# Kernel optimization log

Measured on AMD Instinct MI355X. Metric: run time of the kernel, lower is better.

The kernel has to match this reference:

```python
import jax, jax.numpy as jnp
import numpy as np

GRID_NUM = 5   # number of grid intervals (pykan default)
SPLINE_K = 3   # B-spline degree (pykan default)
GRID_RANGE = (-1.0, 1.0)


def make_grid(in_dim):
    # Extended uniform grid: num + 2k + 1 knots per input dim, shared values.
    h = (GRID_RANGE[1] - GRID_RANGE[0]) / GRID_NUM
    pts = GRID_RANGE[0] + h * jnp.arange(-SPLINE_K, GRID_NUM + SPLINE_K + 1, dtype=jnp.float32)
    return jnp.broadcast_to(pts, (in_dim, pts.shape[0]))  # (in_dim, num+2k+1)


def bspline_basis(x, grid, k):
    # Cox-de Boor recursion. x: (n, d); grid: (d, m). Returns (n, d, m-1-k).
    xe = x[..., None]            # (n, d, 1)
    g = grid[None]               # (1, d, m)
    B = ((xe >= g[..., :-1]) & (xe < g[..., 1:])).astype(x.dtype)
    for p in range(1, k + 1):
        left = (xe - g[..., :-(p + 1)]) / (g[..., p:-1] - g[..., :-(p + 1)])
        right = (g[..., p + 1:] - xe) / (g[..., p + 1:] - g[..., 1:-p])
        B = left * B[..., :-1] + right * B[..., 1:]
    return B


def kan_layer(x, coef, scale_base, scale_sp, grid):
    # x: (n, in); coef: (in, out, G+k); scales: (in, out)
    basis = bspline_basis(x, grid, SPLINE_K)              # (n, in, G+k)
    base = jax.nn.silu(x)                                 # (n, in)
    # y[n,o] = sum_i scale_base[i,o]*silu(x[n,i]) + scale_sp[i,o]*sum_g B[n,i,g]*coef[i,o,g]
    spline = jnp.einsum('nig,iog->no', basis, coef * scale_sp[:, :, None])
    return base @ scale_base + spline


def setup_inputs() -> dict:
    key = jax.random.key(0)
    ks = jax.random.split(key, 5)
    b, s, hid, ffn = 2, 4096, 512, 2048
    nb = GRID_NUM + SPLINE_K  # 8 basis functions
    x = jax.random.normal(ks[0], (b, s, hid), dtype=jnp.float32)
    coef1 = 0.1 * jax.random.normal(ks[1], (hid, ffn, nb), dtype=jnp.float32)
    scale_base1 = (1.0 / np.sqrt(hid)) * jax.random.normal(ks[2], (hid, ffn), dtype=jnp.float32)
    scale_sp1 = jnp.ones((hid, ffn), dtype=jnp.float32)
    coef2 = 0.1 * jax.random.normal(ks[3], (ffn, hid, nb), dtype=jnp.float32)
    scale_base2 = (1.0 / np.sqrt(ffn)) * jax.random.normal(ks[4], (ffn, hid), dtype=jnp.float32)
    scale_sp2 = jnp.ones((ffn, hid), dtype=jnp.float32)
    return {'x': x, 'coef1': coef1, 'scale_base1': scale_base1, 'scale_sp1': scale_sp1,
            'coef2': coef2, 'scale_base2': scale_base2, 'scale_sp2': scale_sp2}


def reference(x, coef1, scale_base1, scale_sp1, coef2, scale_base2, scale_sp2):
    b, s, hid = x.shape
    ffn = coef1.shape[1]
    grid1 = make_grid(hid)   # non-trainable buffers, derived from defaults
    grid2 = make_grid(ffn)
    h = x.reshape(b * s, hid)                     # rearrange 'b s h -> (b s) h'
    h = kan_layer(h, coef1, scale_base1, scale_sp1, grid1)
    h = kan_layer(h, coef2, scale_base2, scale_sp2, grid2)
    return h.reshape(b, s, hid)
```

## Files before the change

### kernel.cpp

```cpp
#include <hip/hip_runtime.h>
#include <cstdint>
#include <cstddef>

typedef _Float16 f16;
typedef _Float16 f16x8 __attribute__((ext_vector_type(8)));
typedef float f32x4 __attribute__((ext_vector_type(4)));


template <int I, int O>
__global__ void prep_coef(const float* __restrict__ coef,
                          const float* __restrict__ ssp,
                          f16* __restrict__ Wt) {
  constexpr int K32 = (9 * I) / 32;
  int tid = blockIdx.x * 256 + threadIdx.x;
  if (tid >= I * O) return;
  int i = tid / O, o = tid % O;
  float s = ssp[tid];
  const float* c = coef + (size_t)tid * 8;
  f16x8 out;
#pragma unroll
  for (int g = 0; g < 8; ++g) out[g] = (f16)(c[g] * s);
  size_t addr = ((size_t)(o >> 4) * K32 + (i >> 2)) * 512 +
                (size_t)(((i & 3) * 16) + (o & 15)) * 8;
  *(f16x8*)(Wt + addr) = out;
}

template <int I, int O>
__global__ void prep_base(const float* __restrict__ sb, f16* __restrict__ Wt) {
  constexpr int K32 = (9 * I) / 32;
  int tid = blockIdx.x * 256 + threadIdx.x;
  if (tid >= (I / 8) * O) return;
  int i8 = tid / O, o = tid % O;
  f16x8 out;
#pragma unroll
  for (int s = 0; s < 8; ++s)
    out[s] = (f16)sb[(size_t)(i8 * 8 + s) * O + o];
  size_t addr = ((size_t)(o >> 4) * K32 + (I / 4) + (i8 >> 2)) * 512 +
                (size_t)(((i8 & 3) * 16) + (o & 15)) * 8;
  *(f16x8*)(Wt + addr) = out;
}

__device__ __forceinline__ f16x8 spline8(float h) {
  float v = __builtin_fmaf(2.5f, h, 5.5f);
  float c = floorf(v);
  float f = v - c;
  float f2 = f * f, f3 = f2 * f;
  float b3 = f3 * (1.f / 6.f);
  float t = 1.f - f;
  float b0 = t * t * t * (1.f / 6.f);
  float b1 = (2.f / 3.f) - f2 + 0.5f * f3;
  float b2 = 1.f - b0 - b1 - b3;
  unsigned int u01 =
      __builtin_bit_cast(unsigned int, __builtin_amdgcn_cvt_pkrtz(b0, b1));
  unsigned int u23 =
      __builtin_bit_cast(unsigned int, __builtin_amdgcn_cvt_pkrtz(b2, b3));
  unsigned long long pk = (unsigned long long)u01 |
                          ((unsigned long long)u23 << 32);
  int ci = (int)c;
  int s = (ci - 3) * 16;
  __uint128_t r = 0;
  if (s >= 0) {
    if (s < 128) r = (__uint128_t)pk << s;
  } else {
    int q = -s;
    if (q < 64) r = (__uint128_t)(pk >> q);
  }
  return __builtin_bit_cast(f16x8, r);
}

template <int I, int ATOMIC, int NX, int NZ>
__global__ __launch_bounds__(256, 2) void gemm_kan(const float* __restrict__ H,
                                                   const f16* __restrict__ W,
                                                   float* __restrict__ C,
                                                   int N) {
  constexpr int K = 9 * I;
  constexpr int KB = 8 * I;
  constexpr int K32 = K / 32;
  constexpr int KSTEP = 64 * NZ;
  constexpr int NSTEP = K / KSTEP;
  __shared__ __align__(16) f16 sA[2 * 128 * 64];
  const int t = threadIdx.x;
  const int wg = blockIdx.x;
  const int pr = wg & 7;
  const int n0 = (pr % NX) * 256;
  const int m0 = (wg >> 3) * 128;
  const int kBeg = (pr / NX) * 64;
  const int w = t >> 6, lane = t & 63;
  const int wm = (w >> 1) * 64, wn = (w & 1) * 128;
  const int lr = lane & 15, lq = lane >> 4;
  const int srow = t >> 3;
  const int j_ = t & 7;
  const int js = j_ ^ (srow & 7);

  f32x4 acc[4][8] = {};
  const float* Hrow = H + (size_t)(m0 + srow) * I;

  float hs[4];

  auto genTile = [&](int kg, f16* wb) {
    if (kg < KB) {
#pragma unroll
      for (int q = 0; q < 4; ++q)
        *(f16x8*)&wb[((q * 32 + srow) * 8 + js) * 8] = spline8(hs[q]);
      const int kn = kg + KSTEP;
      if (kn < KB) {
        const int i0n = kn >> 3;
#pragma unroll
        for (int q = 0; q < 4; ++q)
          hs[q] = Hrow[(size_t)(q * 32) * I + i0n + j_];
      }
    } else {
      const int c0 = (kg - KB) + j_ * 8;
      f32x4 ha[4][2];
#pragma unroll
      for (int q = 0; q < 4; ++q) {
        const f32x4* p = (const f32x4*)(Hrow + (size_t)(q * 32) * I + c0);
        ha[q][0] = p[0];
        ha[q][1] = p[1];
      }
#pragma unroll
      for (int q = 0; q < 4; ++q) {
        f16x8 o;
#pragma unroll
        for (int s = 0; s < 8; ++s) {
          float h = ha[q][s >> 2][s & 3];
          o[s] = (f16)(h / (1.f + __expf(-h)));
        }
        *(f16x8*)&wb[((q * 32 + srow) * 8 + js) * 8] = o;
      }
    }
  };

  if (kBeg < KB) {
    const int i0 = kBeg >> 3;
#pragma unroll
    for (int q = 0; q < 4; ++q)
      hs[q] = Hrow[(size_t)(q * 32) * I + i0 + j_];
  }
  const f16* pk = W + ((size_t)((n0 + wn) >> 4) * K32 + (kBeg >> 5)) * 512 +
                  lane * 8;
  f16x8 bvA[8];
#pragma unroll
  for (int j = 0; j < 8; ++j)
    bvA[j] = *(const f16x8*)(pk + (size_t)j * K32 * 512);
  genTile(kBeg, sA);
  __syncthreads();

  int cur = 0;
  for (int s = 0; s < NSTEP; ++s) {
    const f16* rb = sA + cur * (128 * 64);
    f16* wb = sA + (cur ^ 1) * (128 * 64);

    f16x8 bvB[8];
#pragma unroll
    for (int j = 0; j < 8; ++j)
      bvB[j] = *(const f16x8*)(pk + (size_t)j * K32 * 512 + 512);

    f16x8 av[4];
#pragma unroll
    for (int i = 0; i < 4; ++i) {
      const int ra = wm + i * 16 + lr;
      const int ca = lq ^ (ra & 7);
      av[i] = *(const f16x8*)&rb[ra * 64 + ca * 8];
    }

    __builtin_amdgcn_s_setprio(1);
#pragma unroll
    for (int i = 0; i < 4; ++i)
#pragma unroll
      for (int j = 0; j < 8; ++j)
        acc[i][j] = __builtin_amdgcn_mfma_f32_16x16x32_f16(av[i], bvA[j],
                                                           acc[i][j], 0, 0, 0);
    __builtin_amdgcn_s_setprio(0);

#pragma unroll
    for (int i = 0; i < 4; ++i) {
      const int ra = wm + i * 16 + lr;
      const int ca = (4 + lq) ^ (ra & 7);
      av[i] = *(const f16x8*)&rb[ra * 64 + ca * 8];
    }

    const bool more = (s + 1 < NSTEP);
    if (more) genTile(kBeg + (s + 1) * KSTEP, wb);

    pk += (size_t)(KSTEP / 32) * 512;
    if (more) {
#pragma unroll
      for (int j = 0; j < 8; ++j)
        bvA[j] = *(const f16x8*)(pk + (size_t)j * K32 * 512);
    }

    __builtin_amdgcn_s_setprio(1);
#pragma unroll
    for (int i = 0; i < 4; ++i)
#pragma unroll
      for (int j = 0; j < 8; ++j)
        acc[i][j] = __builtin_amdgcn_mfma_f32_16x16x32_f16(av[i], bvB[j],
                                                           acc[i][j], 0, 0, 0);
    __builtin_amdgcn_s_setprio(0);

    __syncthreads();
    cur ^= 1;
  }

#pragma unroll
  for (int i = 0; i < 4; ++i) {
#pragma unroll
    for (int j = 0; j < 8; ++j) {
      const int col = n0 + wn + j * 16 + lr;
#pragma unroll
      for (int r = 0; r < 4; ++r) {
        const int row = m0 + wm + i * 16 + lq * 4 + r;
        if (ATOMIC)
          atomicAdd(&C[(size_t)row * N + col], acc[i][j][r]);
        else
          C[(size_t)row * N + col] = acc[i][j][r];
      }
    }
  }
}

extern "C" void kernel_launch(void* const* d_in, const int* in_sizes, int n_in,
                              void* d_out, int out_size, void* d_ws,
                              size_t ws_size, hipStream_t stream) {
  const float* x     = (const float*)d_in[0];
  const float* coef1 = (const float*)d_in[1];
  const float* sb1   = (const float*)d_in[2];
  const float* ssp1  = (const float*)d_in[3];
  const float* coef2 = (const float*)d_in[4];
  const float* sb2   = (const float*)d_in[5];
  const float* ssp2  = (const float*)d_in[6];

  const int Mtot = 8192;
  const int I1 = 512, O1 = 2048, K1 = I1 * 9;
  const int I2 = 2048, O2 = 512, K2 = I2 * 9;

  char* ws = (char*)d_ws;
  const size_t szW1 = (size_t)O1 * K1 * sizeof(f16);
  const size_t szW2 = (size_t)O2 * K2 * sizeof(f16);
  const size_t szH  = (size_t)Mtot * O1 * sizeof(float);
  if (ws_size < szW1 + szW2 + szH) return;
  f16*   W1 = (f16*)ws;
  f16*   W2 = (f16*)(ws + szW1);
  float* h1 = (float*)(ws + szW1 + szW2);

  {
    int n1 = I1 * O1;
    prep_coef<512, 2048><<<(n1 + 255) / 256, 256, 0, stream>>>(coef1, ssp1, W1);
    prep_base<512, 2048><<<(n1 / 8 + 255) / 256, 256, 0, stream>>>(sb1, W1);
    int n2 = I2 * O2;
    prep_coef<2048, 512><<<(n2 + 255) / 256, 256, 0, stream>>>(coef2, ssp2, W2);
    prep_base<2048, 512><<<(n2 / 8 + 255) / 256, 256, 0, stream>>>(sb2, W2);
  }

  gemm_kan<512, 0, 8, 1><<<dim3(512), 256, 0, stream>>>(x, W1, h1, O1);

  (void)hipMemsetAsync(d_out, 0, (size_t)Mtot * O2 * sizeof(float), stream);
  gemm_kan<2048, 1, 2, 4><<<dim3(512), 256, 0, stream>>>(h1, W2,
                                                         (float*)d_out, O2);
}
```

Before: 500.2 us.

## Halve GEMM N-tile to 128 and raise occupancy to three blocks per CU

```diff
diff --git a/kernel.cpp b/kernel.cpp
--- a/kernel.cpp
+++ b/kernel.cpp
@@ -69,7 +69,7 @@
 }
 
 template <int I, int ATOMIC, int NX, int NZ>
-__global__ __launch_bounds__(256, 2) void gemm_kan(const float* __restrict__ H,
+__global__ __launch_bounds__(256, 3) void gemm_kan(const float* __restrict__ H,
                                                    const f16* __restrict__ W,
                                                    float* __restrict__ C,
                                                    int N) {
@@ -78,21 +78,23 @@
   constexpr int K32 = K / 32;
   constexpr int KSTEP = 64 * NZ;
   constexpr int NSTEP = K / KSTEP;
+  constexpr int NPAIR = NX * NZ;
   __shared__ __align__(16) f16 sA[2 * 128 * 64];
   const int t = threadIdx.x;
   const int wg = blockIdx.x;
-  const int pr = wg & 7;
-  const int n0 = (pr % NX) * 256;
-  const int m0 = (wg >> 3) * 128;
-  const int kBeg = (pr / NX) * 64;
+  const int pr = wg & (NPAIR - 1);
+  const int z  = pr & (NZ - 1);
+  const int n0 = (pr / NZ) * 128;
+  const int m0 = (wg / NPAIR) * 128;
+  const int kBeg = z * 64;
   const int w = t >> 6, lane = t & 63;
-  const int wm = (w >> 1) * 64, wn = (w & 1) * 128;
+  const int wm = (w >> 1) * 64, wn = (w & 1) * 64;
   const int lr = lane & 15, lq = lane >> 4;
   const int srow = t >> 3;
   const int j_ = t & 7;
   const int js = j_ ^ (srow & 7);
 
-  f32x4 acc[4][8] = {};
+  f32x4 acc[4][4] = {};
   const float* Hrow = H + (size_t)(m0 + srow) * I;
 
   float hs[4];
@@ -139,10 +141,6 @@
   }
   const f16* pk = W + ((size_t)((n0 + wn) >> 4) * K32 + (kBeg >> 5)) * 512 +
                   lane * 8;
-  f16x8 bvA[8];
-#pragma unroll
-  for (int j = 0; j < 8; ++j)
-    bvA[j] = *(const f16x8*)(pk + (size_t)j * K32 * 512);
   genTile(kBeg, sA);
   __syncthreads();
 
@@ -151,10 +149,10 @@
     const f16* rb = sA + cur * (128 * 64);
     f16* wb = sA + (cur ^ 1) * (128 * 64);
 
-    f16x8 bvB[8];
-#pragma unroll
-    for (int j = 0; j < 8; ++j)
-      bvB[j] = *(const f16x8*)(pk + (size_t)j * K32 * 512 + 512);
+    f16x8 bv0[4];
+#pragma unroll
+    for (int j = 0; j < 4; ++j)
+      bv0[j] = *(const f16x8*)(pk + (size_t)j * K32 * 512);
 
     f16x8 av[4];
 #pragma unroll
@@ -164,12 +162,17 @@
       av[i] = *(const f16x8*)&rb[ra * 64 + ca * 8];
     }
 
+    f16x8 bv1[4];
+#pragma unroll
+    for (int j = 0; j < 4; ++j)
+      bv1[j] = *(const f16x8*)(pk + (size_t)j * K32 * 512 + 512);
+
     __builtin_amdgcn_s_setprio(1);
 #pragma unroll
     for (int i = 0; i < 4; ++i)
 #pragma unroll
-      for (int j = 0; j < 8; ++j)
-        acc[i][j] = __builtin_amdgcn_mfma_f32_16x16x32_f16(av[i], bvA[j],
+      for (int j = 0; j < 4; ++j)
+        acc[i][j] = __builtin_amdgcn_mfma_f32_16x16x32_f16(av[i], bv0[j],
                                                            acc[i][j], 0, 0, 0);
     __builtin_amdgcn_s_setprio(0);
 
@@ -180,22 +183,15 @@
       av[i] = *(const f16x8*)&rb[ra * 64 + ca * 8];
     }
 
-    const bool more = (s + 1 < NSTEP);
-    if (more) genTile(kBeg + (s + 1) * KSTEP, wb);
-
+    if (s + 1 < NSTEP) genTile(kBeg + (s + 1) * KSTEP, wb);
     pk += (size_t)(KSTEP / 32) * 512;
-    if (more) {
-#pragma unroll
-      for (int j = 0; j < 8; ++j)
-        bvA[j] = *(const f16x8*)(pk + (size_t)j * K32 * 512);
-    }
 
     __builtin_amdgcn_s_setprio(1);
 #pragma unroll
     for (int i = 0; i < 4; ++i)
 #pragma unroll
-      for (int j = 0; j < 8; ++j)
-        acc[i][j] = __builtin_amdgcn_mfma_f32_16x16x32_f16(av[i], bvB[j],
+      for (int j = 0; j < 4; ++j)
+        acc[i][j] = __builtin_amdgcn_mfma_f32_16x16x32_f16(av[i], bv1[j],
                                                            acc[i][j], 0, 0, 0);
     __builtin_amdgcn_s_setprio(0);
 
@@ -206,7 +202,7 @@
 #pragma unroll
   for (int i = 0; i < 4; ++i) {
 #pragma unroll
-    for (int j = 0; j < 8; ++j) {
+    for (int j = 0; j < 4; ++j) {
       const int col = n0 + wn + j * 16 + lr;
 #pragma unroll
       for (int r = 0; r < 4; ++r) {
@@ -253,9 +249,9 @@
     prep_base<2048, 512><<<(n2 / 8 + 255) / 256, 256, 0, stream>>>(sb2, W2);
   }
 
-  gemm_kan<512, 0, 8, 1><<<dim3(512), 256, 0, stream>>>(x, W1, h1, O1);
+  gemm_kan<512, 0, 16, 1><<<dim3(1024), 256, 0, stream>>>(x, W1, h1, O1);
 
   (void)hipMemsetAsync(d_out, 0, (size_t)Mtot * O2 * sizeof(float), stream);
-  gemm_kan<2048, 1, 2, 4><<<dim3(512), 256, 0, stream>>>(h1, W2,
-                                                         (float*)d_out, O2);
-}
+  gemm_kan<2048, 1, 4, 4><<<dim3(1024), 256, 0, stream>>>(h1, W2,
+                                                          (float*)d_out, O2);
+}
```

Result: slower. 655.0 us (+31.0%).

## Generate A fragments in registers per wave, removing LDS staging and barriers

Applied to the files above, without the earlier changes.

```diff
diff --git a/kernel.cpp b/kernel.cpp
--- a/kernel.cpp
+++ b/kernel.cpp
@@ -78,7 +78,6 @@
   constexpr int K32 = K / 32;
   constexpr int KSTEP = 64 * NZ;
   constexpr int NSTEP = K / KSTEP;
-  __shared__ __align__(16) f16 sA[2 * 128 * 64];
   const int t = threadIdx.x;
   const int wg = blockIdx.x;
   const int pr = wg & 7;
@@ -88,80 +87,69 @@
   const int w = t >> 6, lane = t & 63;
   const int wm = (w >> 1) * 64, wn = (w & 1) * 128;
   const int lr = lane & 15, lq = lane >> 4;
-  const int srow = t >> 3;
-  const int j_ = t & 7;
-  const int js = j_ ^ (srow & 7);
 
   f32x4 acc[4][8] = {};
-  const float* Hrow = H + (size_t)(m0 + srow) * I;
-
-  float hs[4];
-
-  auto genTile = [&](int kg, f16* wb) {
-    if (kg < KB) {
-#pragma unroll
-      for (int q = 0; q < 4; ++q)
-        *(f16x8*)&wb[((q * 32 + srow) * 8 + js) * 8] = spline8(hs[q]);
-      const int kn = kg + KSTEP;
-      if (kn < KB) {
-        const int i0n = kn >> 3;
-#pragma unroll
-        for (int q = 0; q < 4; ++q)
-          hs[q] = Hrow[(size_t)(q * 32) * I + i0n + j_];
-      }
-    } else {
-      const int c0 = (kg - KB) + j_ * 8;
-      f32x4 ha[4][2];
-#pragma unroll
-      for (int q = 0; q < 4; ++q) {
-        const f32x4* p = (const f32x4*)(Hrow + (size_t)(q * 32) * I + c0);
-        ha[q][0] = p[0];
-        ha[q][1] = p[1];
-      }
-#pragma unroll
-      for (int q = 0; q < 4; ++q) {
-        f16x8 o;
-#pragma unroll
-        for (int s = 0; s < 8; ++s) {
-          float h = ha[q][s >> 2][s & 3];
-          o[s] = (f16)(h / (1.f + __expf(-h)));
-        }
-        *(f16x8*)&wb[((q * 32 + srow) * 8 + js) * 8] = o;
-      }
-    }
-  };
-
-  if (kBeg < KB) {
-    const int i0 = kBeg >> 3;
-#pragma unroll
-    for (int q = 0; q < 4; ++q)
-      hs[q] = Hrow[(size_t)(q * 32) * I + i0 + j_];
-  }
+
+  const float* Hf[4];
+#pragma unroll
+  for (int f = 0; f < 4; ++f)
+    Hf[f] = H + (size_t)(m0 + wm + f * 16 + lr) * I;
+
   const f16* pk = W + ((size_t)((n0 + wn) >> 4) * K32 + (kBeg >> 5)) * 512 +
                   lane * 8;
+
+  float hc[4][2];
+  {
+    const int i0 = kBeg >> 3;
+#pragma unroll
+    for (int f = 0; f < 4; ++f)
+#pragma unroll
+      for (int h = 0; h < 2; ++h)
+        hc[f][h] = Hf[f][i0 + h * 4 + lq];
+  }
   f16x8 bvA[8];
 #pragma unroll
   for (int j = 0; j < 8; ++j)
     bvA[j] = *(const f16x8*)(pk + (size_t)j * K32 * 512);
-  genTile(kBeg, sA);
-  __syncthreads();
-
-  int cur = 0;
+
   for (int s = 0; s < NSTEP; ++s) {
-    const f16* rb = sA + cur * (128 * 64);
-    f16* wb = sA + (cur ^ 1) * (128 * 64);
+    const int k0 = kBeg + s * KSTEP;
 
     f16x8 bvB[8];
 #pragma unroll
     for (int j = 0; j < 8; ++j)
       bvB[j] = *(const f16x8*)(pk + (size_t)j * K32 * 512 + 512);
 
+    const int k0n = k0 + KSTEP;
+    const bool nsp = (s + 1 < NSTEP) && (k0n < KB);
+    float hn[4][2];
+    if (nsp) {
+      const int in0 = k0n >> 3;
+#pragma unroll
+      for (int f = 0; f < 4; ++f)
+#pragma unroll
+        for (int h = 0; h < 2; ++h)
+          hn[f][h] = Hf[f][in0 + h * 4 + lq];
+    }
+
     f16x8 av[4];
-#pragma unroll
-    for (int i = 0; i < 4; ++i) {
-      const int ra = wm + i * 16 + lr;
-      const int ca = lq ^ (ra & 7);
-      av[i] = *(const f16x8*)&rb[ra * 64 + ca * 8];
+    if (k0 < KB) {
+#pragma unroll
+      for (int f = 0; f < 4; ++f) av[f] = spline8(hc[f][0]);
+    } else {
+      const int cc = (k0 - KB) + lq * 8;
+#pragma unroll
+      for (int f = 0; f < 4; ++f) {
+        const f32x4* p = (const f32x4*)(Hf[f] + cc);
+        f32x4 a0 = p[0], a1 = p[1];
+        f16x8 o;
+#pragma unroll
+        for (int j = 0; j < 8; ++j) {
+          float h = (j < 4) ? a0[j & 3] : a1[j & 3];
+          o[j] = (f16)(h / (1.f + __expf(-h)));
+        }
+        av[f] = o;
+      }
     }
 
     __builtin_amdgcn_s_setprio(1);
@@ -173,18 +161,27 @@
                                                            acc[i][j], 0, 0, 0);
     __builtin_amdgcn_s_setprio(0);
 
-#pragma unroll
-    for (int i = 0; i < 4; ++i) {
-      const int ra = wm + i * 16 + lr;
-      const int ca = (4 + lq) ^ (ra & 7);
-      av[i] = *(const f16x8*)&rb[ra * 64 + ca * 8];
-    }
-
-    const bool more = (s + 1 < NSTEP);
-    if (more) genTile(kBeg + (s + 1) * KSTEP, wb);
+    if (k0 < KB) {
+#pragma unroll
+      for (int f = 0; f < 4; ++f) av[f] = spline8(hc[f][1]);
+    } else {
+      const int cc = (k0 - KB) + 32 + lq * 8;
+#pragma unroll
+      for (int f = 0; f < 4; ++f) {
+        const f32x4* p = (const f32x4*)(Hf[f] + cc);
+        f32x4 a0 = p[0], a1 = p[1];
+        f16x8 o;
+#pragma unroll
+        for (int j = 0; j < 8; ++j) {
+          float h = (j < 4) ? a0[j & 3] : a1[j & 3];
+          o[j] = (f16)(h / (1.f + __expf(-h)));
+        }
+        av[f] = o;
+      }
+    }
 
     pk += (size_t)(KSTEP / 32) * 512;
-    if (more) {
+    if (s + 1 < NSTEP) {
 #pragma unroll
       for (int j = 0; j < 8; ++j)
         bvA[j] = *(const f16x8*)(pk + (size_t)j * K32 * 512);
@@ -199,8 +196,13 @@
                                                            acc[i][j], 0, 0, 0);
     __builtin_amdgcn_s_setprio(0);
 
-    __syncthreads();
-    cur ^= 1;
+    if (nsp) {
+#pragma unroll
+      for (int f = 0; f < 4; ++f)
+#pragma unroll
+        for (int h = 0; h < 2; ++h)
+          hc[f][h] = hn[f][h];
+    }
   }
 
 #pragma unroll
```

New measurement: 794.6 us. +58.9%, slower.

## Give each wave a private A tile and drop block-wide barriers

Applied to the files above, without the earlier changes.

```diff
diff --git a/kernel.cpp b/kernel.cpp
--- a/kernel.cpp
+++ b/kernel.cpp
@@ -78,7 +78,8 @@
   constexpr int K32 = K / 32;
   constexpr int KSTEP = 64 * NZ;
   constexpr int NSTEP = K / KSTEP;
-  __shared__ __align__(16) f16 sA[2 * 128 * 64];
+  constexpr int BUF = 4 * 64 * 64;
+  __shared__ __align__(16) f16 sA[2 * BUF];
   const int t = threadIdx.x;
   const int wg = blockIdx.x;
   const int pr = wg & 7;
@@ -88,54 +89,51 @@
   const int w = t >> 6, lane = t & 63;
   const int wm = (w >> 1) * 64, wn = (w & 1) * 128;
   const int lr = lane & 15, lq = lane >> 4;
-  const int srow = t >> 3;
-  const int j_ = t & 7;
-  const int js = j_ ^ (srow & 7);
+  const int r_ = lane >> 3;
+  const int j_ = lane & 7;
+  const int js = j_ ^ r_;
+
+  f16* myA = sA + w * (64 * 64);
 
   f32x4 acc[4][8] = {};
-  const float* Hrow = H + (size_t)(m0 + srow) * I;
-
-  float hs[4];
+  const float* Hg = H + (size_t)(m0 + wm + r_) * I;
+
+  float hs[8];
 
   auto genTile = [&](int kg, f16* wb) {
     if (kg < KB) {
 #pragma unroll
-      for (int q = 0; q < 4; ++q)
-        *(f16x8*)&wb[((q * 32 + srow) * 8 + js) * 8] = spline8(hs[q]);
+      for (int q = 0; q < 8; ++q)
+        *(f16x8*)&wb[(q * 8 + r_) * 64 + js * 8] = spline8(hs[q]);
       const int kn = kg + KSTEP;
       if (kn < KB) {
         const int i0n = kn >> 3;
 #pragma unroll
-        for (int q = 0; q < 4; ++q)
-          hs[q] = Hrow[(size_t)(q * 32) * I + i0n + j_];
+        for (int q = 0; q < 8; ++q)
+          hs[q] = Hg[(size_t)(q * 8) * I + i0n + j_];
       }
     } else {
       const int c0 = (kg - KB) + j_ * 8;
-      f32x4 ha[4][2];
-#pragma unroll
-      for (int q = 0; q < 4; ++q) {
-        const f32x4* p = (const f32x4*)(Hrow + (size_t)(q * 32) * I + c0);
-        ha[q][0] = p[0];
-        ha[q][1] = p[1];
+#pragma unroll
+      for (int q = 0; q < 8; ++q) {
+        const f32x4* p = (const f32x4*)(Hg + (size_t)(q * 8) * I + c0);
+        f32x4 a0 = p[0], a1 = p[1];
+        f16x8 o;
+#pragma unroll
+        for (int e = 0; e < 8; ++e) {
+          float h = (e < 4) ? a0[e & 3] : a1[e & 3];
+          o[e] = (f16)(h / (1.f + __expf(-h)));
+        }
+        *(f16x8*)&wb[(q * 8 + r_) * 64 + js * 8] = o;
       }
-#pragma unroll
-      for (int q = 0; q < 4; ++q) {
-        f16x8 o;
-#pragma unroll
-        for (int s = 0; s < 8; ++s) {
-          float h = ha[q][s >> 2][s & 3];
-          o[s] = (f16)(h / (1.f + __expf(-h)));
-        }
-        *(f16x8*)&wb[((q * 32 + srow) * 8 + js) * 8] = o;
-      }
     }
   };
 
-  if (kBeg < KB) {
+  {
     const int i0 = kBeg >> 3;
 #pragma unroll
-    for (int q = 0; q < 4; ++q)
-      hs[q] = Hrow[(size_t)(q * 32) * I + i0 + j_];
+    for (int q = 0; q < 8; ++q)
+      hs[q] = Hg[(size_t)(q * 8) * I + i0 + j_];
   }
   const f16* pk = W + ((size_t)((n0 + wn) >> 4) * K32 + (kBeg >> 5)) * 512 +
                   lane * 8;
@@ -143,13 +141,12 @@
 #pragma unroll
   for (int j = 0; j < 8; ++j)
     bvA[j] = *(const f16x8*)(pk + (size_t)j * K32 * 512);
-  genTile(kBeg, sA);
-  __syncthreads();
+  genTile(kBeg, myA);
 
   int cur = 0;
   for (int s = 0; s < NSTEP; ++s) {
-    const f16* rb = sA + cur * (128 * 64);
-    f16* wb = sA + (cur ^ 1) * (128 * 64);
+    const f16* rb = myA + cur * BUF;
+    f16* wb = myA + (cur ^ 1) * BUF;
 
     f16x8 bvB[8];
 #pragma unroll
@@ -159,7 +156,7 @@
     f16x8 av[4];
 #pragma unroll
     for (int i = 0; i < 4; ++i) {
-      const int ra = wm + i * 16 + lr;
+      const int ra = i * 16 + lr;
       const int ca = lq ^ (ra & 7);
       av[i] = *(const f16x8*)&rb[ra * 64 + ca * 8];
     }
@@ -175,7 +172,7 @@
 
 #pragma unroll
     for (int i = 0; i < 4; ++i) {
-      const int ra = wm + i * 16 + lr;
+      const int ra = i * 16 + lr;
       const int ca = (4 + lq) ^ (ra & 7);
       av[i] = *(const f16x8*)&rb[ra * 64 + ca * 8];
     }
@@ -199,7 +196,6 @@
                                                            acc[i][j], 0, 0, 0);
     __builtin_amdgcn_s_setprio(0);
 
-    __syncthreads();
     cur ^= 1;
   }
 
```

New measurement: 606.9 us. +21.3%, slower.
